# Optimization experiments

Hardware: AMD Instinct MI355X
Metric: run time of the kernel (lower is better)

The kernel has to match this reference:

```python
import jax, jax.numpy as jnp
import numpy as np

B, T = 1024, 48
NA, NM = 35, 18
N = NA + NM
H = 32            # hid_dim / out_features
CTX = 60          # context feature dim per node
D = H + CTX       # per-node attention feature dim (92); 2*D+1 = 185 = 2*H+121
ALPHA = 0.2
NEG = -1e12


def _leaky(x):
    return jnp.where(x >= 0, x, ALPHA * x)


def _gru(x, h, wih, whh, bih, bhh):
    # torch.nn.GRUCell math, gate order (r, z, n)
    gi = x @ wih.T + bih
    gh = h @ whh.T + bhh
    ir, iz, i_n = jnp.split(gi, 3, axis=-1)
    hr, hz, h_n = jnp.split(gh, 3, axis=-1)
    r = jax.nn.sigmoid(ir + hr)
    z = jax.nn.sigmoid(iz + hz)
    n = jnp.tanh(i_n + r * h_n)
    return (1.0 - z) * n + z * h


def setup_inputs() -> dict:
    key = jax.random.key(0)
    ks = iter(jax.random.split(key, 64))
    rn = lambda shp, s=0.1: jax.random.normal(next(ks), shp, jnp.float32) * s
    inp = dict(
        X_aqi=rn((B, T, NA, 6), 1.0),
        X_meo=rn((B, T, NM, 4), 1.0),
        context_feat=rn((N, CTX), 1.0),
        adj=(jax.random.uniform(next(ks), (N, N)) > 0.3).astype(jnp.float32),
        adj_norm=jax.random.uniform(next(ks), (N, N)),
        emb_aqi_id=rn((35, 2)), emb_aqi_month=rn((13, 2)),
        emb_aqi_weekday=rn((7, 2)), emb_aqi_hour=rn((24, 2)),
        emb_meo_wind=rn((9, 2)), emb_meo_id=rn((18, 2)),
        emb_meo_month=rn((13, 2)), emb_meo_weekday=rn((7, 2)),
        emb_meo_hour=rn((24, 2)),
        W_xa=rn((6, H)), W_xm=rn((4, H)),
        W_ua=rn((14, H)), W_um=rn((14, H)),
        a_aa=rn((2 * D + 1,)), a_am=rn((2 * D + 1,)),
        a_ma=rn((2 * D + 1,)), a_mm=rn((2 * D + 1,)),
        gru_aqi_wih=rn((3 * H, H)), gru_aqi_whh=rn((3 * H, H)),
        gru_aqi_bih=rn((3 * H,)), gru_aqi_bhh=rn((3 * H,)),
        gru_meo_wih=rn((3 * H, H)), gru_meo_whh=rn((3 * H, H)),
        gru_meo_bih=rn((3 * H,)), gru_meo_bhh=rn((3 * H,)),
        X_aqi_ex=jax.random.randint(next(ks), (B, T, NA, 4), 0, 7),
        X_meo_ex=jax.random.randint(next(ks), (B, T, NM, 5), 0, 7),
    )
    return inp


def _forward(X_aqi, X_meo, context_feat, adj, adj_norm,
             emb_aqi_id, emb_aqi_month, emb_aqi_weekday, emb_aqi_hour,
             emb_meo_wind, emb_meo_id, emb_meo_month, emb_meo_weekday, emb_meo_hour,
             W_xa, W_xm, W_ua, W_um, a_aa, a_am, a_ma, a_mm,
             gru_aqi_wih, gru_aqi_whh, gru_aqi_bih, gru_aqi_bhh,
             gru_meo_wih, gru_meo_whh, gru_meo_bih, gru_meo_bhh,
             X_aqi_ex, X_meo_ex):
    b = X_aqi.shape[0]
    mask = adj > 0
    sA, sM = slice(0, NA), slice(NA, N)

    def chgat(aqi_x, meo_x, aqi_ex, meo_ex):
        # attribute transform on raw features only -> aggregation values
        attri = jnp.concatenate([aqi_x @ W_xa, meo_x @ W_xm], axis=1)      # [B,N,H]
        aqi_in = jnp.concatenate([aqi_x,
                                  emb_aqi_id[aqi_ex[..., 0]],
                                  emb_aqi_month[aqi_ex[..., 1]],
                                  emb_aqi_weekday[aqi_ex[..., 2]],
                                  emb_aqi_hour[aqi_ex[..., 3]]], axis=-1)   # [B,NA,14]
        meo_in = jnp.concatenate([meo_x,
                                  emb_meo_wind[meo_ex[..., 0]],
                                  emb_meo_id[meo_ex[..., 1]],
                                  emb_meo_month[meo_ex[..., 2]],
                                  emb_meo_weekday[meo_ex[..., 3]],
                                  emb_meo_hour[meo_ex[..., 4]]], axis=-1)   # [B,NM,14]
        feat = jnp.concatenate([aqi_in @ W_ua, meo_in @ W_um], axis=1)      # [B,N,H]
        feat = jnp.concatenate(
            [feat, jnp.broadcast_to(context_feat, (b, N, CTX))], axis=-1)   # [B,N,D]

        # e_ij = leakyrelu([f_i | f_j | adj_norm_ij] @ a); split a to avoid
        # materializing the original [B,N,N,2D+1] tensor
        def e_block(a, rs, cs):
            src = feat[:, rs] @ a[:D]           # [B,nr]
            dst = feat[:, cs] @ a[D:2 * D]      # [B,nc]
            return _leaky(src[:, :, None] + dst[:, None, :]
                          + adj_norm[rs, cs] * a[2 * D])

        e = jnp.concatenate([
            jnp.concatenate([e_block(a_aa, sA, sA), e_block(a_am, sA, sM)], axis=2),
            jnp.concatenate([e_block(a_ma, sM, sA), e_block(a_mm, sM, sM)], axis=2),
        ], axis=1)                                                          # [B,N,N]
        att = jax.nn.softmax(jnp.where(mask, e, NEG), axis=2)
        out = att @ attri                                                   # [B,N,H]
        return out[:, :NA], out[:, NA:]

    def step(carry, xs):
        h_aqi, h_meo = carry
        ax, mx, ae, me = xs
        fa, fm = chgat(ax, mx, ae, me)
        h_aqi = _gru(fa.reshape(-1, H), h_aqi.reshape(-1, H),
                     gru_aqi_wih, gru_aqi_whh, gru_aqi_bih, gru_aqi_bhh).reshape(b, NA, H)
        h_meo = _gru(fm.reshape(-1, H), h_meo.reshape(-1, H),
                     gru_meo_wih, gru_meo_whh, gru_meo_bih, gru_meo_bhh).reshape(b, NM, H)
        return (h_aqi, h_meo), None

    init = (jnp.zeros((b, NA, H), X_aqi.dtype), jnp.zeros((b, NM, H), X_aqi.dtype))
    xs = (jnp.moveaxis(X_aqi, 1, 0), jnp.moveaxis(X_meo, 1, 0),
          jnp.moveaxis(X_aqi_ex, 1, 0), jnp.moveaxis(X_meo_ex, 1, 0))
    (h_aqi, h_meo), _ = jax.lax.scan(step, init, xs)
    return h_aqi, h_meo


def reference(X_aqi, X_meo, context_feat, adj, adj_norm,
              emb_aqi_id, emb_aqi_month, emb_aqi_weekday, emb_aqi_hour,
              emb_meo_wind, emb_meo_id, emb_meo_month, emb_meo_weekday, emb_meo_hour,
              W_xa, W_xm, W_ua, W_um, a_aa, a_am, a_ma, a_mm,
              gru_aqi_wih, gru_aqi_whh, gru_aqi_bih, gru_aqi_bhh,
              gru_meo_wih, gru_meo_whh, gru_meo_bih, gru_meo_bhh,
              X_aqi_ex, X_meo_ex):
    return _forward(X_aqi, X_meo, context_feat, adj, adj_norm,
                    emb_aqi_id, emb_aqi_month, emb_aqi_weekday, emb_aqi_hour,
                    emb_meo_wind, emb_meo_id, emb_meo_month, emb_meo_weekday, emb_meo_hour,
                    W_xa, W_xm, W_ua, W_um, a_aa, a_am, a_ma, a_mm,
                    gru_aqi_wih, gru_aqi_whh, gru_aqi_bih, gru_aqi_bhh,
                    gru_meo_wih, gru_meo_whh, gru_meo_bih, gru_meo_bhh,
                    X_aqi_ex, X_meo_ex)
```

## Files before the change

### kernel.cpp

```cpp
#include <hip/hip_runtime.h>
#include <hip/hip_bf16.h>

#define NA 35
#define NM 18
#define NN 53
#define TT 48
#define HH 32
#define OUT_MEO_BASE (1024*35*32)
#define XHS 72

typedef unsigned short u16;
typedef __attribute__((ext_vector_type(8))) short s8v;
typedef __attribute__((ext_vector_type(4))) float f4v;

__device__ __forceinline__ float bfu(u16 u){ return __uint_as_float(((unsigned)u)<<16); }
__device__ __forceinline__ u16 cvtbf(float f){
  unsigned u = __float_as_uint(f);
  return (u16)((u + 0x7FFFu + ((u>>16)&1u)) >> 16);
}

struct Params {
  const void *X_aqi, *X_meo, *ctx, *adj, *adjn;
  const void *emb0,*emb1,*emb2,*emb3,*emb4,*emb5,*emb6,*emb7,*emb8;
  const void *Wxa,*Wxm,*Wua,*Wum;
  const void *a0,*a1,*a2,*a3;
  const void *wih_a,*whh_a,*bih_a,*bhh_a,*wih_m,*whh_m,*bih_m,*bhh_m;
  const int *Xae,*Xme;
  void* out;
};

__device__ __forceinline__ float ldf(const void* p, int i, bool isbf){
  return isbf ? bfu(((const u16*)p)[i]) : ((const float*)p)[i];
}
__device__ __forceinline__ u16 ldraw(const void* p, int i, bool isbf){
  return isbf ? ((const u16*)p)[i] : cvtbf(((const float*)p)[i]);
}

struct __align__(16) BatchState {
  alignas(16) float xin[NN*16];
  alignas(16) u16   xinbf[64*32];
  alignas(16) u16   afrag[4*64*8];
  alignas(16) float srcv[NN*2], dstv[NN*2];
  alignas(16) u16   pbf[64*XHS];
  alignas(16) float inv[56];
  alignas(16) u16   xh[64*XHS];
  alignas(16) float h[NN*32];
};

struct __align__(16) Smem {
  alignas(16) float gb[4][96];
  alignas(16) float embA[304];
  alignas(16) float ctxS[NN][2], ctxD[NN][2];
  alignas(16) float uSrc[2][2][14];
  alignas(16) float uDst[2][2][14];
  alignas(16) u16   biasE[NN*56];
  alignas(16) u16   wfA[2*64*8];
  alignas(16) u16   wfrag[2*12*64*8];
  BatchState bs[2];
};

__global__ __launch_bounds__(512)
void chgat_gru_kernel(Params p){
  __shared__ Smem sm;
  const int tid = threadIdx.x;
  const int bid = blockIdx.x;

  bool isbf = false;
  {
    const unsigned* aw = (const unsigned*)p.adj;
    for (int i=0;i<32;++i){
      unsigned w = aw[i];
      if (w != 0u && w != 0x3F800000u) isbf = true;
    }
  }
  auto aPtr = [&](int s)->const void*{
    return s==0 ? p.a0 : s==1 ? p.a1 : s==2 ? p.a2 : p.a3;
  };

  if (tid < 96){
    sm.gb[0][tid]=ldf(p.bih_a,tid,isbf); sm.gb[1][tid]=ldf(p.bhh_a,tid,isbf);
    sm.gb[2][tid]=ldf(p.bih_m,tid,isbf); sm.gb[3][tid]=ldf(p.bhh_m,tid,isbf);
  }
  if (tid < 70)  sm.embA[tid]        = ldf(p.emb0, tid, isbf);
  if (tid < 26)  sm.embA[70+tid]     = ldf(p.emb1, tid, isbf);
  if (tid < 14)  sm.embA[96+tid]     = ldf(p.emb2, tid, isbf);
  if (tid < 48)  sm.embA[110+tid]    = ldf(p.emb3, tid, isbf);
  if (tid < 18)  sm.embA[158+tid]    = ldf(p.emb4, tid, isbf);
  if (tid < 36)  sm.embA[176+tid]    = ldf(p.emb5, tid, isbf);
  if (tid < 26)  sm.embA[212+tid]    = ldf(p.emb6, tid, isbf);
  if (tid < 14)  sm.embA[238+tid]    = ldf(p.emb7, tid, isbf);
  if (tid < 48)  sm.embA[252+tid]    = ldf(p.emb8, tid, isbf);
  for (int idx=tid; idx<2*NN*32; idx+=512) sm.bs[idx/(NN*32)].h[idx%(NN*32)] = 0.f;
  for (int idx=tid; idx<2*64*XHS; idx+=512) sm.bs[idx/(64*XHS)].xh[idx%(64*XHS)] = 0;
  for (int idx=tid; idx<2*64*XHS; idx+=512) sm.bs[idx/(64*XHS)].pbf[idx%(64*XHS)] = 0;
  for (int idx=tid; idx<2*4*64*8; idx+=512) sm.bs[idx/(4*64*8)].afrag[idx%(4*64*8)] = 0;
  for (int idx=tid; idx<2*64*32; idx+=512) sm.bs[idx/(64*32)].xinbf[idx%(64*32)] = 0;
  if (tid < 128){
    int l = tid & 63, nl2 = l & 15, qd2 = l >> 4, nt = tid >> 6;
    u16* dst = &sm.wfA[tid*8];
    #pragma unroll
    for (int j=0;j<8;++j){
      int k = qd2*8 + j, n = nt*16 + nl2;
      u16 v = 0;
      if (k < 6)              v = ldraw(p.Wxa, k*32+n, isbf);
      else if (k>=8 && k<12)  v = ldraw(p.Wxm, (k-8)*32+n, isbf);
      dst[j] = v;
    }
  }
  for (int u = tid; u < 2*12*64; u += 512){
    int wty2 = u / (12*64);
    int rem  = u - wty2*(12*64);
    int f = rem >> 6, l = rem & 63;
    int nl2 = l & 15, qd2 = l >> 4;
    const void* W = (f < 6) ? (wty2 ? p.wih_m : p.wih_a) : (wty2 ? p.whh_m : p.whh_a);
    int fr = (f < 6) ? f : f - 6;
    int base = (fr*16 + nl2)*32 + qd2*8;
    u16* dst = &sm.wfrag[u*8];
    #pragma unroll
    for (int j=0;j<8;++j) dst[j] = ldraw(W, base+j, isbf);
  }
  __syncthreads();

  if (tid < 212){
    int i = tid>>2, v = tid&3, it = (i<NA)?0:1;
    int sel = (v<2) ? (it*2+v) : ((v-2)*2+it);
    int off = (v<2) ? 32 : 124;
    const void* ap = aPtr(sel);
    float s = 0.f;
    for (int c=0;c<60;++c) s += ldf(p.ctx, i*60+c, isbf)*ldf(ap, off+c, isbf);
    if (v < 2) sm.ctxS[i][v] = s; else sm.ctxD[i][v-2] = s;
  }
  if (tid < 112){
    int u = tid;
    int it = u / 56, rem = u % 56;
    int sd = rem / 28, rem2 = rem % 28;
    int v = rem2 / 14, k = rem2 % 14;
    const void* Wu = it ? p.Wum : p.Wua;
    int sel = sd ? (v*2+it) : (it*2+v);
    int off = sd ? 92 : 0;
    const void* ap = aPtr(sel);
    float s = 0.f;
    for (int kk=0;kk<32;++kk) s += ldf(Wu, k*32+kk, isbf)*ldf(ap, off+kk, isbf);
    if (sd) sm.uDst[it][v][k] = s; else sm.uSrc[it][v][k] = s;
  }
  for (int idx=tid; idx<NN*NN; idx+=512){
    int i = idx/NN, j = idx - i*NN;
    int sel = ((i<NA)?0:2) + ((j<NA)?0:1);
    float ad = ldf(p.adj, idx, isbf);
    sm.biasE[i*56+j] = cvtbf((ad > 0.f) ? ldf(p.adjn, idx, isbf)*ldf(aPtr(sel),184,isbf) : -1e12f);
  }
  __syncthreads();

  const int hb   = tid >> 8;
  const int lt   = tid & 255;
  const int lw   = lt >> 6;
  const int lane = tid & 63;
  const int nl   = lane & 15;
  const int qd   = lane >> 4;
  const int bb   = 2*bid + hb;

  BatchState& st = sm.bs[hb];
  const int wty = (lw==3) ? 1 : 0;
  const s8v* wfB = ((const s8v*)sm.wfrag) + (wty*12*64 + lane);

  float rv1 = 0.f, rv2r = 0.f; int rv2i = 0;
  {
    int bt = bb*TT + 0;
    rv1 = (lt < 210) ? ldf(p.X_aqi, bt*210 + lt, isbf) : ldf(p.X_meo, bt*72 + lt - 210, isbf);
    if (lt < 26) rv2r = ldf(p.X_meo, bt*72 + lt + 46, isbf);
    else { int u = lt - 26; rv2i = (u < 140) ? p.Xae[bt*140 + u] : p.Xme[bt*90 + u - 140]; }
  }

  #pragma unroll 1
  for (int t=0; t<TT; ++t){
    if (lt < 210){
      int n = lt/6, e = lt%6;
      st.xin[n*16 + e] = rv1;
      st.xinbf[n*32 + e] = cvtbf(rv1);
    } else {
      int q = lt-210; int n = NA + (q>>2), e = q&3;
      st.xin[n*16 + e] = rv1;
      st.xinbf[n*32 + 8 + e] = cvtbf(rv1);
    }
    if (lt < 26){
      int q = lt + 46; int n = NA + (q>>2), e = q&3;
      st.xin[n*16 + e] = rv2r;
      st.xinbf[n*32 + 8 + e] = cvtbf(rv2r);
    } else {
      int u = lt - 26;
      if (u < 140){
        int n = u>>2, e = u&3;
        int off = (e==0)?0:(e==1)?70:(e==2)?96:110;
        st.xin[n*16 + 6 + 2*e]     = sm.embA[off + rv2i*2];
        st.xin[n*16 + 6 + 2*e + 1] = sm.embA[off + rv2i*2 + 1];
      } else {
        int q = u - 140;
        int n = NA + q/5, e = q%5;
        int off = (e==0)?158:(e==1)?176:(e==2)?212:(e==3)?238:252;
        st.xin[n*16 + 4 + 2*e]     = sm.embA[off + rv2i*2];
        st.xin[n*16 + 4 + 2*e + 1] = sm.embA[off + rv2i*2 + 1];
      }
    }
    {
      int tn = (t < TT-1) ? t+1 : t;
      int bt = bb*TT + tn;
      rv1 = (lt < 210) ? ldf(p.X_aqi, bt*210 + lt, isbf) : ldf(p.X_meo, bt*72 + lt - 210, isbf);
      if (lt < 26) rv2r = ldf(p.X_meo, bt*72 + lt + 46, isbf);
      else { int u = lt - 26; rv2i = (u < 140) ? p.Xae[bt*140 + u] : p.Xme[bt*90 + u - 140]; }
    }
    __syncthreads();

    {
      s8v A0 = *(const s8v*)&st.xinbf[(lw*16 + nl)*32 + qd*8];
      #pragma unroll 1
      for (int nt=0; nt<2; ++nt){
        s8v B0 = ((const s8v*)sm.wfA)[nt*64 + lane];
        f4v acc = {0,0,0,0};
        acc = __builtin_amdgcn_mfma_f32_16x16x32_bf16(A0, B0, acc, 0,0,0);
        #pragma unroll
        for (int r=0;r<4;++r){
          int row = lw*16 + qd*4 + r;
          if (row < NN){
            int fi = ((row>>5)*2 + nt)*64 + (nl + (((row>>3)&3)<<4));
            st.afrag[fi*8 + (row&7)] = cvtbf(acc[r]);
          }
        }
      }
    }
    if (lt < 212){
      int i = lt>>2, v = lt&3, it2 = (i<NA)?0:1;
      const float* x = &st.xin[i*16];
      float sacc; const float* uv;
      if (v < 2){ sacc = sm.ctxS[i][v];   uv = sm.uSrc[it2][v]; }
      else      { sacc = sm.ctxD[i][v-2]; uv = sm.uDst[it2][v-2]; }
      #pragma unroll
      for (int k=0;k<14;++k) sacc += x[k]*uv[k];
      if (v < 2) st.srcv[i*2+v] = sacc; else st.dstv[i*2+(v-2)] = sacc;
    }
    __syncthreads();

    if (lt < 212){
      int i = lt>>2, l = lt&3, it2 = (i<NA)?0:1;
      float s0 = st.srcv[i*2+0], s1 = st.srcv[i*2+1];
      float mx = -3.0e38f;
      for (int j=l; j<NN; j+=4){
        float e = ((j<NA)? s0 : s1) + st.dstv[j*2+it2] + bfu(sm.biasE[i*56+j]);
        e = (e >= 0.f) ? e : 0.2f*e;
        mx = fmaxf(mx, e);
      }
      mx = fmaxf(mx, __shfl_xor(mx,1,64));
      mx = fmaxf(mx, __shfl_xor(mx,2,64));
      float sum = 0.f;
      for (int j=l; j<NN; j+=4){
        float e = ((j<NA)? s0 : s1) + st.dstv[j*2+it2] + bfu(sm.biasE[i*56+j]);
        e = (e >= 0.f) ? e : 0.2f*e;
        float pe = __expf(e - mx);
        st.pbf[i*XHS+j] = cvtbf(pe);
        sum += pe;
      }
      sum += __shfl_xor(sum,1,64);
      sum += __shfl_xor(sum,2,64);
      if (l == 0) st.inv[i] = 1.0f/sum;
    }
    __syncthreads();

    {
      const u16* arow = &st.pbf[(lw*16 + nl)*XHS + qd*8];
      s8v A0 = *(const s8v*)arow;
      s8v A1 = *(const s8v*)(arow + 32);
      const s8v* bf = (const s8v*)st.afrag;
      #pragma unroll 1
      for (int nt=0; nt<2; ++nt){
        s8v B0 = bf[(0*2+nt)*64 + lane];
        s8v B1 = bf[(1*2+nt)*64 + lane];
        f4v acc = {0,0,0,0};
        acc = __builtin_amdgcn_mfma_f32_16x16x32_bf16(A0, B0, acc, 0,0,0);
        acc = __builtin_amdgcn_mfma_f32_16x16x32_bf16(A1, B1, acc, 0,0,0);
        const int dcol = nt*16 + nl;
        #pragma unroll
        for (int r=0;r<4;++r){
          int row = lw*16 + qd*4 + r;
          if (row < NN) st.xh[row*XHS + dcol] = cvtbf(acc[r] * st.inv[row]);
        }
      }
    }
    __syncthreads();

    {
      const bool last = (t == TT-1);
      auto run_pass = [&](int mt, int tp){
        const u16* xr = &st.xh[(mt*16 + nl)*XHS + qd*8];
        s8v A0 = *(const s8v*)xr;
        s8v A1 = *(const s8v*)(xr + 32);
        const float* bi = tp ? sm.gb[2] : sm.gb[0];
        const float* bh = tp ? sm.gb[3] : sm.gb[1];
        #pragma unroll 1
        for (int hf=0; hf<2; ++hf){
          f4v aR={0,0,0,0}, aZ={0,0,0,0}, aI={0,0,0,0}, aG={0,0,0,0};
          aR = __builtin_amdgcn_mfma_f32_16x16x32_bf16(A0, wfB[(0+hf)*64],  aR, 0,0,0);
          aR = __builtin_amdgcn_mfma_f32_16x16x32_bf16(A1, wfB[(6+hf)*64],  aR, 0,0,0);
          aZ = __builtin_amdgcn_mfma_f32_16x16x32_bf16(A0, wfB[(2+hf)*64],  aZ, 0,0,0);
          aZ = __builtin_amdgcn_mfma_f32_16x16x32_bf16(A1, wfB[(8+hf)*64],  aZ, 0,0,0);
          aI = __builtin_amdgcn_mfma_f32_16x16x32_bf16(A0, wfB[(4+hf)*64],  aI, 0,0,0);
          aG = __builtin_amdgcn_mfma_f32_16x16x32_bf16(A1, wfB[(10+hf)*64], aG, 0,0,0);
          const int dd = nl + hf*16;
          float br=bi[dd]+bh[dd], bz=bi[32+dd]+bh[32+dd], bn=bi[64+dd], bg=bh[64+dd];
          #pragma unroll
          for (int r=0;r<4;++r){
            int node = mt*16 + qd*4 + r;
            bool valid = tp ? (node>=NA && node<NN) : (node<NA);
            if (valid){
              float hold = st.h[node*32+dd];
              float rr = 1.f/(1.f+__expf(-(aR[r]+br)));
              float zz = 1.f/(1.f+__expf(-(aZ[r]+bz)));
              float pr = (aI[r]+bn) + rr*(aG[r]+bg);
              float e2 = __expf(2.f*pr);
              float hn = (1.f-zz)*(1.f-2.f/(e2+1.f)) + zz*hold;
              st.h[node*32+dd] = hn;
              st.xh[node*XHS+32+dd] = cvtbf(hn);
              if (last){
                long long oi = tp ? ((long long)OUT_MEO_BASE + (long long)bb*(NM*HH) + (long long)(node-NA)*32)
                                  : ((long long)bb*(NA*HH) + (long long)node*32);
                if (isbf) ((u16*)p.out)[oi+dd]=cvtbf(hn);
                else      ((float*)p.out)[oi+dd]=hn;
              }
            }
          }
        }
      };
      if (lw < 3) run_pass(lw, 0);
      else { run_pass(2,1); run_pass(3,1); }
    }
  }
}

extern "C" void kernel_launch(void* const* d_in, const int* in_sizes, int n_in,
                              void* d_out, int out_size, void* d_ws, size_t ws_size,
                              hipStream_t stream){
  (void)in_sizes; (void)n_in; (void)d_ws; (void)ws_size; (void)out_size;
  Params p;
  p.X_aqi = d_in[0];
  p.X_meo = d_in[1];
  p.ctx   = d_in[2];
  p.adj   = d_in[3];
  p.adjn  = d_in[4];
  p.emb0 = d_in[5];  p.emb1 = d_in[6];
  p.emb2 = d_in[7];  p.emb3 = d_in[8];
  p.emb4 = d_in[9];  p.emb5 = d_in[10];
  p.emb6 = d_in[11]; p.emb7 = d_in[12];
  p.emb8 = d_in[13];
  p.Wxa = d_in[14]; p.Wxm = d_in[15];
  p.Wua = d_in[16]; p.Wum = d_in[17];
  p.a0 = d_in[18]; p.a1 = d_in[19];
  p.a2 = d_in[20]; p.a3 = d_in[21];
  p.wih_a = d_in[22]; p.whh_a = d_in[23];
  p.bih_a = d_in[24]; p.bhh_a = d_in[25];
  p.wih_m = d_in[26]; p.whh_m = d_in[27];
  p.bih_m = d_in[28]; p.bhh_m = d_in[29];
  p.Xae = (const int*)d_in[30];
  p.Xme = (const int*)d_in[31];
  p.out = d_out;
  hipLaunchKernelGGL(chgat_gru_kernel, dim3(512), dim3(512), 0, stream, p);
}
```

Baseline: 994.4 us.

## Pack four batches per block with two waves each and alias scratch buffers

Each 512-thread block now handles four batch elements with 128 threads (two waves) each instead of two with 256 threads, and the grid is halved to 256 blocks. Per-batch scratch (xin, xinbf, pbf) is merged into one aliased buffer so four batch states fit in shared memory, and xinbf padding is re-zeroed every step. Each wave takes on more MFMA tiles, softmax rows and GRU passes in sequence, aiming to make better use of waves per CU and of the fixed setup cost. The trade-off is less parallelism inside each batch, longer serial work per wave, and 256 blocks that may not fill all CUs.

```diff
diff --git a/kernel.cpp b/kernel.cpp
--- a/kernel.cpp
+++ b/kernel.cpp
@@ -37,11 +37,9 @@
 }
 
 struct __align__(16) BatchState {
-  alignas(16) float xin[NN*16];
-  alignas(16) u16   xinbf[64*32];
+  alignas(16) u16   uni[64*XHS];
   alignas(16) u16   afrag[4*64*8];
   alignas(16) float srcv[NN*2], dstv[NN*2];
-  alignas(16) u16   pbf[64*XHS];
   alignas(16) float inv[56];
   alignas(16) u16   xh[64*XHS];
   alignas(16) float h[NN*32];
@@ -56,7 +54,7 @@
   alignas(16) u16   biasE[NN*56];
   alignas(16) u16   wfA[2*64*8];
   alignas(16) u16   wfrag[2*12*64*8];
-  BatchState bs[2];
+  BatchState bs[4];
 };
 
 __global__ __launch_bounds__(512)
@@ -90,11 +88,10 @@
   if (tid < 26)  sm.embA[212+tid]    = ldf(p.emb6, tid, isbf);
   if (tid < 14)  sm.embA[238+tid]    = ldf(p.emb7, tid, isbf);
   if (tid < 48)  sm.embA[252+tid]    = ldf(p.emb8, tid, isbf);
-  for (int idx=tid; idx<2*NN*32; idx+=512) sm.bs[idx/(NN*32)].h[idx%(NN*32)] = 0.f;
-  for (int idx=tid; idx<2*64*XHS; idx+=512) sm.bs[idx/(64*XHS)].xh[idx%(64*XHS)] = 0;
-  for (int idx=tid; idx<2*64*XHS; idx+=512) sm.bs[idx/(64*XHS)].pbf[idx%(64*XHS)] = 0;
-  for (int idx=tid; idx<2*4*64*8; idx+=512) sm.bs[idx/(4*64*8)].afrag[idx%(4*64*8)] = 0;
-  for (int idx=tid; idx<2*64*32; idx+=512) sm.bs[idx/(64*32)].xinbf[idx%(64*32)] = 0;
+  for (int idx=tid; idx<4*64*XHS; idx+=512) sm.bs[idx/(64*XHS)].uni[idx%(64*XHS)] = 0;
+  for (int idx=tid; idx<4*64*XHS; idx+=512) sm.bs[idx/(64*XHS)].xh[idx%(64*XHS)] = 0;
+  for (int idx=tid; idx<4*4*64*8; idx+=512) sm.bs[idx/(4*64*8)].afrag[idx%(4*64*8)] = 0;
+  for (int idx=tid; idx<4*NN*32; idx+=512) sm.bs[idx/(NN*32)].h[idx%(NN*32)] = 0.f;
   if (tid < 128){
     int l = tid & 63, nl2 = l & 15, qd2 = l >> 4, nt = tid >> 6;
     u16* dst = &sm.wfA[tid*8];
@@ -151,85 +148,109 @@
   }
   __syncthreads();
 
-  const int hb   = tid >> 8;
-  const int lt   = tid & 255;
+  const int hb   = tid >> 7;
+  const int lt   = tid & 127;
   const int lw   = lt >> 6;
   const int lane = tid & 63;
   const int nl   = lane & 15;
   const int qd   = lane >> 4;
-  const int bb   = 2*bid + hb;
+  const int bb   = 4*bid + hb;
 
   BatchState& st = sm.bs[hb];
-  const int wty = (lw==3) ? 1 : 0;
-  const s8v* wfB = ((const s8v*)sm.wfrag) + (wty*12*64 + lane);
-
-  float rv1 = 0.f, rv2r = 0.f; int rv2i = 0;
+  u16*   pbf   = st.uni;
+  float* xin   = reinterpret_cast<float*>(st.uni);
+  u16*   xinbf = st.uni + 1696;
+
+  auto pref = [&](int slot, int bt)->unsigned{
+    if (slot < 210) return __float_as_uint(ldf(p.X_aqi, bt*210 + slot, isbf));
+    if (slot < 282) return __float_as_uint(ldf(p.X_meo, bt*72 + slot - 210, isbf));
+    if (slot < 422) return (unsigned)p.Xae[bt*140 + slot - 282];
+    return (unsigned)p.Xme[bt*90 + slot - 422];
+  };
+  auto scat = [&](int slot, unsigned bits){
+    if (slot < 210){
+      int n = slot/6, e = slot%6;
+      float v = __uint_as_float(bits);
+      xin[n*16 + e] = v;
+      xinbf[n*32 + e] = cvtbf(v);
+    } else if (slot < 282){
+      int q = slot-210; int n = NA + (q>>2), e = q&3;
+      float v = __uint_as_float(bits);
+      xin[n*16 + e] = v;
+      xinbf[n*32 + 8 + e] = cvtbf(v);
+    } else if (slot < 422){
+      int u = slot - 282;
+      int n = u>>2, e = u&3;
+      int off = (e==0)?0:(e==1)?70:(e==2)?96:110;
+      xin[n*16 + 6 + 2*e]     = sm.embA[off + (int)bits*2];
+      xin[n*16 + 6 + 2*e + 1] = sm.embA[off + (int)bits*2 + 1];
+    } else {
+      int q = slot - 422;
+      int n = NA + q/5, e = q%5;
+      int off = (e==0)?158:(e==1)?176:(e==2)?212:(e==3)?238:252;
+      xin[n*16 + 4 + 2*e]     = sm.embA[off + (int)bits*2];
+      xin[n*16 + 4 + 2*e + 1] = sm.embA[off + (int)bits*2 + 1];
+    }
+  };
+
+  unsigned rv0, rv1, rv2, rv3;
   {
     int bt = bb*TT + 0;
-    rv1 = (lt < 210) ? ldf(p.X_aqi, bt*210 + lt, isbf) : ldf(p.X_meo, bt*72 + lt - 210, isbf);
-    if (lt < 26) rv2r = ldf(p.X_meo, bt*72 + lt + 46, isbf);
-    else { int u = lt - 26; rv2i = (u < 140) ? p.Xae[bt*140 + u] : p.Xme[bt*90 + u - 140]; }
+    rv0 = pref(lt      , bt);
+    rv1 = pref(lt + 128, bt);
+    rv2 = pref(lt + 256, bt);
+    rv3 = pref(lt + 384, bt);
   }
 
   #pragma unroll 1
   for (int t=0; t<TT; ++t){
-    if (lt < 210){
-      int n = lt/6, e = lt%6;
-      st.xin[n*16 + e] = rv1;
-      st.xinbf[n*32 + e] = cvtbf(rv1);
-    } else {
-      int q = lt-210; int n = NA + (q>>2), e = q&3;
-      st.xin[n*16 + e] = rv1;
-      st.xinbf[n*32 + 8 + e] = cvtbf(rv1);
-    }
-    if (lt < 26){
-      int q = lt + 46; int n = NA + (q>>2), e = q&3;
-      st.xin[n*16 + e] = rv2r;
-      st.xinbf[n*32 + 8 + e] = cvtbf(rv2r);
-    } else {
-      int u = lt - 26;
-      if (u < 140){
-        int n = u>>2, e = u&3;
-        int off = (e==0)?0:(e==1)?70:(e==2)?96:110;
-        st.xin[n*16 + 6 + 2*e]     = sm.embA[off + rv2i*2];
-        st.xin[n*16 + 6 + 2*e + 1] = sm.embA[off + rv2i*2 + 1];
-      } else {
-        int q = u - 140;
-        int n = NA + q/5, e = q%5;
-        int off = (e==0)?158:(e==1)?176:(e==2)?212:(e==3)?238:252;
-        st.xin[n*16 + 4 + 2*e]     = sm.embA[off + rv2i*2];
-        st.xin[n*16 + 4 + 2*e + 1] = sm.embA[off + rv2i*2 + 1];
+    scat(lt      , rv0);
+    scat(lt + 128, rv1);
+    scat(lt + 256, rv2);
+    scat(lt + 384, rv3);
+    {
+      int row = lt >> 1, c0 = (lt & 1) * 16;
+      #pragma unroll
+      for (int c = 0; c < 16; ++c){
+        int col = c0 + c;
+        bool isval = (row < NA) ? (col < 6) : (row < NN ? (col >= 8 && col < 12) : false);
+        if (!isval) xinbf[row*32 + col] = 0;
       }
     }
     {
       int tn = (t < TT-1) ? t+1 : t;
       int bt = bb*TT + tn;
-      rv1 = (lt < 210) ? ldf(p.X_aqi, bt*210 + lt, isbf) : ldf(p.X_meo, bt*72 + lt - 210, isbf);
-      if (lt < 26) rv2r = ldf(p.X_meo, bt*72 + lt + 46, isbf);
-      else { int u = lt - 26; rv2i = (u < 140) ? p.Xae[bt*140 + u] : p.Xme[bt*90 + u - 140]; }
+      rv0 = pref(lt      , bt);
+      rv1 = pref(lt + 128, bt);
+      rv2 = pref(lt + 256, bt);
+      rv3 = pref(lt + 384, bt);
     }
     __syncthreads();
 
     {
-      s8v A0 = *(const s8v*)&st.xinbf[(lw*16 + nl)*32 + qd*8];
       #pragma unroll 1
-      for (int nt=0; nt<2; ++nt){
-        s8v B0 = ((const s8v*)sm.wfA)[nt*64 + lane];
-        f4v acc = {0,0,0,0};
-        acc = __builtin_amdgcn_mfma_f32_16x16x32_bf16(A0, B0, acc, 0,0,0);
-        #pragma unroll
-        for (int r=0;r<4;++r){
-          int row = lw*16 + qd*4 + r;
-          if (row < NN){
-            int fi = ((row>>5)*2 + nt)*64 + (nl + (((row>>3)&3)<<4));
-            st.afrag[fi*8 + (row&7)] = cvtbf(acc[r]);
+      for (int mi=0; mi<2; ++mi){
+        int mt = lw*2 + mi;
+        s8v A0 = *(const s8v*)&xinbf[(mt*16 + nl)*32 + qd*8];
+        #pragma unroll 1
+        for (int nt=0; nt<2; ++nt){
+          s8v B0 = ((const s8v*)sm.wfA)[nt*64 + lane];
+          f4v acc = {0,0,0,0};
+          acc = __builtin_amdgcn_mfma_f32_16x16x32_bf16(A0, B0, acc, 0,0,0);
+          #pragma unroll
+          for (int r=0;r<4;++r){
+            int row = mt*16 + qd*4 + r;
+            if (row < NN){
+              int fi = ((row>>5)*2 + nt)*64 + (nl + (((row>>3)&3)<<4));
+              st.afrag[fi*8 + (row&7)] = cvtbf(acc[r]);
+            }
           }
         }
       }
     }
-    if (lt < 212){
-      int i = lt>>2, v = lt&3, it2 = (i<NA)?0:1;
-      const float* x = &st.xin[i*16];
+    for (int it = lt; it < 212; it += 128){
+      int i = it>>2, v = it&3, it2 = (i<NA)?0:1;
+      const float* x = &xin[i*16];
       float sacc; const float* uv;
       if (v < 2){ sacc = sm.ctxS[i][v];   uv = sm.uSrc[it2][v]; }
       else      { sacc = sm.ctxD[i][v-2]; uv = sm.uDst[it2][v-2]; }
@@ -239,48 +260,51 @@
     }
     __syncthreads();
 
-    if (lt < 212){
-      int i = lt>>2, l = lt&3, it2 = (i<NA)?0:1;
+    if (lt < 106){
+      int i = lt>>1, l = lt&1, it2 = (i<NA)?0:1;
       float s0 = st.srcv[i*2+0], s1 = st.srcv[i*2+1];
       float mx = -3.0e38f;
-      for (int j=l; j<NN; j+=4){
+      for (int j=l; j<NN; j+=2){
         float e = ((j<NA)? s0 : s1) + st.dstv[j*2+it2] + bfu(sm.biasE[i*56+j]);
         e = (e >= 0.f) ? e : 0.2f*e;
         mx = fmaxf(mx, e);
       }
       mx = fmaxf(mx, __shfl_xor(mx,1,64));
-      mx = fmaxf(mx, __shfl_xor(mx,2,64));
       float sum = 0.f;
-      for (int j=l; j<NN; j+=4){
+      for (int j=l; j<NN; j+=2){
         float e = ((j<NA)? s0 : s1) + st.dstv[j*2+it2] + bfu(sm.biasE[i*56+j]);
         e = (e >= 0.f) ? e : 0.2f*e;
         float pe = __expf(e - mx);
-        st.pbf[i*XHS+j] = cvtbf(pe);
+        pbf[i*XHS+j] = cvtbf(pe);
         sum += pe;
       }
       sum += __shfl_xor(sum,1,64);
-      sum += __shfl_xor(sum,2,64);
       if (l == 0) st.inv[i] = 1.0f/sum;
+      for (int j2 = 53+l; j2 < 64; j2 += 2) pbf[i*XHS+j2] = 0;
     }
     __syncthreads();
 
     {
-      const u16* arow = &st.pbf[(lw*16 + nl)*XHS + qd*8];
-      s8v A0 = *(const s8v*)arow;
-      s8v A1 = *(const s8v*)(arow + 32);
-      const s8v* bf = (const s8v*)st.afrag;
       #pragma unroll 1
-      for (int nt=0; nt<2; ++nt){
-        s8v B0 = bf[(0*2+nt)*64 + lane];
-        s8v B1 = bf[(1*2+nt)*64 + lane];
-        f4v acc = {0,0,0,0};
-        acc = __builtin_amdgcn_mfma_f32_16x16x32_bf16(A0, B0, acc, 0,0,0);
-        acc = __builtin_amdgcn_mfma_f32_16x16x32_bf16(A1, B1, acc, 0,0,0);
-        const int dcol = nt*16 + nl;
-        #pragma unroll
-        for (int r=0;r<4;++r){
-          int row = lw*16 + qd*4 + r;
-          if (row < NN) st.xh[row*XHS + dcol] = cvtbf(acc[r] * st.inv[row]);
+      for (int mi=0; mi<2; ++mi){
+        int mt = lw*2 + mi;
+        const u16* arow = &pbf[(mt*16 + nl)*XHS + qd*8];
+        s8v A0 = *(const s8v*)arow;
+        s8v A1 = *(const s8v*)(arow + 32);
+        const s8v* bf = (const s8v*)st.afrag;
+        #pragma unroll 1
+        for (int nt=0; nt<2; ++nt){
+          s8v B0 = bf[(0*2+nt)*64 + lane];
+          s8v B1 = bf[(1*2+nt)*64 + lane];
+          f4v acc = {0,0,0,0};
+          acc = __builtin_amdgcn_mfma_f32_16x16x32_bf16(A0, B0, acc, 0,0,0);
+          acc = __builtin_amdgcn_mfma_f32_16x16x32_bf16(A1, B1, acc, 0,0,0);
+          const int dcol = nt*16 + nl;
+          #pragma unroll
+          for (int r=0;r<4;++r){
+            int row = mt*16 + qd*4 + r;
+            if (row < NN) st.xh[row*XHS + dcol] = cvtbf(acc[r] * st.inv[row]);
+          }
         }
       }
     }
@@ -289,6 +313,7 @@
     {
       const bool last = (t == TT-1);
       auto run_pass = [&](int mt, int tp){
+        const s8v* wfB = ((const s8v*)sm.wfrag) + (tp*12*64 + lane);
         const u16* xr = &st.xh[(mt*16 + nl)*XHS + qd*8];
         s8v A0 = *(const s8v*)xr;
         s8v A1 = *(const s8v*)(xr + 32);
@@ -328,8 +353,8 @@
           }
         }
       };
-      if (lw < 3) run_pass(lw, 0);
-      else { run_pass(2,1); run_pass(3,1); }
+      if (lw == 0){ run_pass(0,0); run_pass(1,0); }
+      else        { run_pass(2,0); run_pass(2,1); run_pass(3,1); }
     }
   }
 }
@@ -360,5 +385,5 @@
   p.Xae = (const int*)d_in[30];
   p.Xme = (const int*)d_in[31];
   p.out = d_out;
-  hipLaunchKernelGGL(chgat_gru_kernel, dim3(512), dim3(512), 0, stream, p);
-}
+  hipLaunchKernelGGL(chgat_gru_kernel, dim3(256), dim3(512), 0, stream, p);
+}
```

Result: faster. 862.9 us (-13.2%).
